# Kernel optimization log

Measured on AMD Instinct MI355X. Metric: run time of the kernel, lower is better.

## Reference

```python
import jax, jax.numpy as jnp
import numpy as np
import math

B, S, D = 8, 4096, 768
H = 12
DH = D // H  # attention_head_size = 64


def setup_inputs() -> dict:
    key = jax.random.key(0)
    ks = jax.random.split(key, 6)
    sc = 0.02
    return {
        "hidden_states": jax.random.normal(ks[0], (B, S, D), dtype=jnp.float32),
        "attention_mask": jnp.zeros((B, 1, S), dtype=jnp.float32),
        "Wq": jax.random.normal(ks[1], (D, D), dtype=jnp.float32) * sc,
        "bq": jnp.zeros((D,), dtype=jnp.float32),
        "Wqa": jax.random.normal(ks[2], (H, D), dtype=jnp.float32) * sc,
        "bqa": jnp.zeros((H,), dtype=jnp.float32),
        "Wk": jax.random.normal(ks[3], (D, D), dtype=jnp.float32) * sc,
        "bk": jnp.zeros((D,), dtype=jnp.float32),
        "Wt": jax.random.normal(ks[4], (D, D), dtype=jnp.float32) * sc,
        "bt": jnp.zeros((D,), dtype=jnp.float32),
    }


def reference(hidden_states, attention_mask, Wq, bq, Wqa, bqa, Wk, bk, Wt, bt):
    inv_sqrt_dh = 1.0 / math.sqrt(DH)
    # projections (torch nn.Linear: x @ W.T + b)
    q = hidden_states @ Wq.T + bq            # [B,S,D]
    k = hidden_states @ Wk.T + bk            # [B,S,D]
    # query attention logits -> [B,H,S]
    qfs = jnp.swapaxes(q @ Wqa.T + bqa, 1, 2) * inv_sqrt_dh + attention_mask
    qw = jax.nn.softmax(qfs, axis=-1)        # [B,H,S]
    ql = jnp.swapaxes(q.reshape(B, S, H, DH), 1, 2)  # [B,H,S,DH]
    kl = jnp.swapaxes(k.reshape(B, S, H, DH), 1, 2)  # [B,H,S,DH]
    # global pooled query per head
    pooled_q = jnp.einsum('bhs,bhsd->bhd', qw, ql)   # [B,H,DH]
    # key attention over pooled query
    qks = jnp.einsum('bhsd,bhd->bhs', kl, pooled_q) * inv_sqrt_dh + attention_mask
    qkw = jax.nn.softmax(qks, axis=-1)       # [B,H,S]
    pooled_k = jnp.einsum('bhs,bhsd->bhd', qkw, kl)  # [B,H,DH]
    # gate query with pooled key, merge heads
    wv = pooled_k[:, :, None, :] * ql        # [B,H,S,DH]
    wv = jnp.swapaxes(wv, 1, 2).reshape(B, S, D)
    return wv @ Wt.T + bt + q
```

## Files before the change

kernel.cpp:

```cpp
#include <hip/hip_runtime.h>
#include <cstdint>
#include <cstddef>

#define S_LEN 4096
#define NB 8
#define NH 12
#define DMODEL 768
#define DHEAD 64
#define M_TOT (NB * S_LEN)
#define INV_SQRT_DH 0.125f
#define WSZ (DMODEL * DMODEL)

typedef __attribute__((ext_vector_type(4))) float f32x4;
typedef __attribute__((ext_vector_type(8))) short bf16x8;

__device__ inline float bf2f(unsigned short h) {
    union { unsigned int u; float f; } v; v.u = ((unsigned int)h) << 16; return v.f;
}
__device__ inline unsigned short f2bf(float f) {
    union { float f; unsigned int u; } v; v.f = f;
    unsigned int r = v.u + 0x7FFFu + ((v.u >> 16) & 1u);
    return (unsigned short)(r >> 16);
}

__device__ inline void gload_lds16(const unsigned short* gp, void* lp) {
    __builtin_amdgcn_global_load_lds((const __attribute__((address_space(1))) void*)gp,
                                     (__attribute__((address_space(3))) void*)lp,
                                     16, 0, 0);
}

__global__ void prep_all(const float* __restrict__ hs,
                         const float* __restrict__ Wq, const float* __restrict__ Wk,
                         const float* __restrict__ Wt, const float* __restrict__ Wqa,
                         const float* __restrict__ bq, const float* __restrict__ bk,
                         unsigned short* __restrict__ hs_bf,
                         unsigned short* __restrict__ Wqk_bf, unsigned short* __restrict__ Wt_bf,
                         unsigned short* __restrict__ Wqa_bf, float* __restrict__ bqk) {
    int bid = blockIdx.x;
    int t = threadIdx.x;
    if (bid < 24576) {
        int off = bid * 1024 + t * 4;
        float4 v = *(const float4*)(hs + off);
        ushort4 o;
        o.x = f2bf(v.x); o.y = f2bf(v.y); o.z = f2bf(v.z); o.w = f2bf(v.w);
        *(ushort4*)(hs_bf + off) = o;
        return;
    }
    bid -= 24576;
    if (bid < 1728) {
        const float* src = (bid < 576) ? Wq : ((bid < 1152) ? Wk : Wt);
        unsigned short* dst = (bid < 576) ? Wqk_bf : ((bid < 1152) ? (Wqk_bf + WSZ) : Wt_bf);
        int off = (bid % 576) * 1024 + t * 4;
        float4 v = *(const float4*)(src + off);
        ushort4 o;
        o.x = f2bf(v.x); o.y = f2bf(v.y); o.z = f2bf(v.z); o.w = f2bf(v.w);
        *(ushort4*)(dst + off) = o;
    } else if (bid < 1740) {
        int off = (bid - 1728) * 1024 + t * 4;
        int h = off / DMODEL;
        ushort4 o = {0, 0, 0, 0};
        if (h < NH) {
            float4 v = *(const float4*)(Wqa + off);
            o.x = f2bf(v.x); o.y = f2bf(v.y); o.z = f2bf(v.z); o.w = f2bf(v.w);
        }
        *(ushort4*)(Wqa_bf + off) = o;
    } else {
        int off = (bid - 1740) * 1024 + t * 4;
        if (off < 2 * DMODEL) {
            const float* src = (off < DMODEL) ? (bq + off) : (bk + off - DMODEL);
            *(float4*)(bqk + off) = *(const float4*)src;
        }
    }
}

#define PH_MID() do { __builtin_amdgcn_s_barrier(); \
    asm volatile("s_waitcnt lgkmcnt(0)"); \
    __builtin_amdgcn_sched_barrier(0); \
    __builtin_amdgcn_s_setprio(1); } while (0)
#define PH_END() do { __builtin_amdgcn_s_setprio(0); \
    __builtin_amdgcn_s_barrier(); } while (0)

#define STG_A(q, kt, BO) gload_lds16(pA + (size_t)((q) * 64) * 768 + (kt) * 64, \
                                     lds + (BO) + (q) * 8192 + wOff)
#define STG_B(q, kt, BO) gload_lds16(pB + (size_t)((q) * 64) * 768 + (kt) * 64, \
                                     lds + (BO) + 32768 + (q) * 8192 + wOff)

#define LD_A(mh, BO) do { _Pragma("unroll") for (int mm = 0; mm < 4; ++mm) { \
    a[mm][0] = *(const bf16x8*)(lds + (BO) + aRd0 + ((mh) * 4 + mm) * 2048); \
    a[mm][1] = *(const bf16x8*)(lds + (BO) + aRd1 + ((mh) * 4 + mm) * 2048); } } while (0)
#define LD_B(nh, BO) do { _Pragma("unroll") for (int nn = 0; nn < 2; ++nn) { \
    b[(nh) * 2 + nn][0] = *(const bf16x8*)(lds + (BO) + bRd0 + ((nh) * 2 + nn) * 2048); \
    b[(nh) * 2 + nn][1] = *(const bf16x8*)(lds + (BO) + bRd1 + ((nh) * 2 + nn) * 2048); } } while (0)
#define MFMAQ(mh, nh) do { _Pragma("unroll") for (int mm = 0; mm < 4; ++mm) \
    _Pragma("unroll") for (int nn = 0; nn < 2; ++nn) { \
        acc[(mh) * 4 + mm][(nh) * 2 + nn] = __builtin_amdgcn_mfma_f32_16x16x32_bf16( \
            a[mm][0], b[(nh) * 2 + nn][0], acc[(mh) * 4 + mm][(nh) * 2 + nn], 0, 0, 0); \
        acc[(mh) * 4 + mm][(nh) * 2 + nn] = __builtin_amdgcn_mfma_f32_16x16x32_bf16( \
            a[mm][1], b[(nh) * 2 + nn][1], acc[(mh) * 4 + mm][(nh) * 2 + nn], 0, 0, 0); } } while (0)

__global__ __launch_bounds__(512, 2) void gemm8(
    const unsigned short* __restrict__ A,
    const unsigned short* __restrict__ Bw,
    const float* __restrict__ bias,
    unsigned short* __restrict__ outBf, int ldoBf,
    int ntn)
{
    __shared__ __align__(16) char lds[131072];

    int nwg = gridDim.x;
    int bid = blockIdx.x;
    int cpx = nwg >> 3;
    int swz = (bid & 7) * cpx + (bid >> 3);
    int bidn = swz % ntn, bidm = swz / ntn;
    int m0 = bidm * 256, n0 = bidn * 256;

    int t = threadIdx.x;
    int w = t >> 6, lane = t & 63;
    int lr = lane & 15, lk = lane >> 4;
    int wr = w >> 2, wc = w & 3;
    int wOff = w << 10;

    int srow = t >> 3;
    int sblk = (t & 7) ^ (srow & 7);
    const unsigned short* pA = A + (size_t)(m0 + srow) * 768 + sblk * 8;
    const unsigned short* pB = Bw + (size_t)(n0 + srow) * 768 + sblk * 8;

    int sx = lr & 7;
    int aRd0 = (wr * 128 + lr) * 128 + ((0 + lk) ^ sx) * 16;
    int aRd1 = (wr * 128 + lr) * 128 + ((4 + lk) ^ sx) * 16;
    int bRd0 = 32768 + (wc * 64 + lr) * 128 + ((0 + lk) ^ sx) * 16;
    int bRd1 = 32768 + (wc * 64 + lr) * 128 + ((4 + lk) ^ sx) * 16;

    f32x4 acc[8][4];
#pragma unroll
    for (int m = 0; m < 8; ++m)
#pragma unroll
        for (int n = 0; n < 4; ++n)
            acc[m][n] = (f32x4){0.f, 0.f, 0.f, 0.f};
    bf16x8 a[4][2], b[4][2];

    STG_A(0, 0, 0); STG_A(1, 0, 0); STG_A(2, 0, 0); STG_A(3, 0, 0);
    STG_B(0, 0, 0); STG_B(1, 0, 0); STG_B(2, 0, 0); STG_B(3, 0, 0);
    STG_A(0, 1, 65536); STG_A(2, 1, 65536);
    STG_B(0, 1, 65536); STG_B(1, 1, 65536); STG_B(2, 1, 65536); STG_B(3, 1, 65536);
    asm volatile("s_waitcnt vmcnt(6)");
    __builtin_amdgcn_s_barrier();

    for (int i = 0; i < 6; ++i) {
        int ktE = 2 * i, ktO = 2 * i + 1;
        int s2 = (i < 5);
        LD_A(0, 0); LD_B(0, 0);
        STG_A(1, ktO, 65536); STG_A(3, ktO, 65536);
        PH_MID(); MFMAQ(0, 0); PH_END();
        LD_B(1, 0);
        if (s2) { STG_A(0, ktE + 2, 0); STG_A(2, ktE + 2, 0); }
        PH_MID(); MFMAQ(0, 1); PH_END();
        LD_A(1, 0);
        if (s2) { STG_B(0, ktE + 2, 0); STG_B(1, ktE + 2, 0); }
        PH_MID(); MFMAQ(1, 1); PH_END();
        if (s2) { STG_B(2, ktE + 2, 0); STG_B(3, ktE + 2, 0); }
        PH_MID(); MFMAQ(1, 0);
        __builtin_amdgcn_s_setprio(0);
        if (s2) { asm volatile("s_waitcnt vmcnt(6)"); }
        else    { asm volatile("s_waitcnt vmcnt(0)"); }
        __builtin_amdgcn_s_barrier();
        LD_A(0, 65536); LD_B(0, 65536);
        if (s2) { STG_A(1, ktE + 2, 0); STG_A(3, ktE + 2, 0); }
        PH_MID(); MFMAQ(0, 0); PH_END();
        LD_B(1, 65536);
        if (s2) { STG_A(0, ktO + 2, 65536); STG_A(2, ktO + 2, 65536); }
        PH_MID(); MFMAQ(0, 1); PH_END();
        LD_A(1, 65536);
        if (s2) { STG_B(0, ktO + 2, 65536); STG_B(1, ktO + 2, 65536); }
        PH_MID(); MFMAQ(1, 1); PH_END();
        if (s2) { STG_B(2, ktO + 2, 65536); STG_B(3, ktO + 2, 65536); }
        PH_MID(); MFMAQ(1, 0);
        __builtin_amdgcn_s_setprio(0);
        if (s2) { asm volatile("s_waitcnt vmcnt(6)"); }
        __builtin_amdgcn_s_barrier();
    }

#pragma unroll
    for (int m = 0; m < 8; ++m) {
        int gr0 = m0 + wr * 128 + m * 16 + lk * 4;
#pragma unroll
        for (int n = 0; n < 4; ++n) {
            int gc = n0 + wc * 64 + n * 16 + lr;
            float bv = bias[gc];
#pragma unroll
            for (int r = 0; r < 4; ++r) {
                int gr = gr0 + r;
                outBf[(size_t)gr * ldoBf + gc] = f2bf(acc[m][n][r] + bv);
            }
        }
    }
}

#define STG3_A(q, kt, BO) gload_lds16(pA + (size_t)((q) * 64) * 1536 + (kt) * 64, \
                                      lds + (BO) + (q) * 8192 + wOff)
#define STG3_B(q, kt, BO) gload_lds16(pB + (size_t)((q) * 64) * 768 + (kt) * 64, \
                                      lds + (BO) + 32768 + (q) * 8192 + wOff)
#define LD3_A(mlo, BO) do { _Pragma("unroll") for (int mm = 0; mm < 4; ++mm) { \
    a[mm][0] = *(const bf16x8*)(lds + (BO) + aRd0 + ((mlo) + mm) * 2048); \
    a[mm][1] = *(const bf16x8*)(lds + (BO) + aRd1 + ((mlo) + mm) * 2048); } } while (0)
#define LD3_B(BO) do { _Pragma("unroll") for (int nn = 0; nn < 2; ++nn) { \
    b[nn][0] = *(const bf16x8*)(lds + (BO) + bRd0 + (nn) * 2048); \
    b[nn][1] = *(const bf16x8*)(lds + (BO) + bRd1 + (nn) * 2048); } } while (0)
#define MFMA3(mlo) do { _Pragma("unroll") for (int mm = 0; mm < 4; ++mm) \
    _Pragma("unroll") for (int nn = 0; nn < 2; ++nn) { \
        acc[(mlo) + mm][nn] = __builtin_amdgcn_mfma_f32_16x16x32_bf16( \
            a[mm][0], b[nn][0], acc[(mlo) + mm][nn], 0, 0, 0); \
        acc[(mlo) + mm][nn] = __builtin_amdgcn_mfma_f32_16x16x32_bf16( \
            a[mm][1], b[nn][1], acc[(mlo) + mm][nn], 0, 0, 0); } } while (0)

#define TILE3(t, BO, SO) do { \
    int t2 = (t) + 2; int s2 = (t2 < 12); \
    LD3_A(0, BO); LD3_B(BO); \
    if (s2) { STG3_A(0, t2, SO); STG3_A(1, t2, SO); STG3_A(2, t2, SO); } \
    PH_MID(); MFMA3(0); PH_END(); \
    LD3_A(4, BO); \
    if (s2) { STG3_A(3, t2, SO); STG3_B(0, t2, SO); STG3_B(1, t2, SO); } \
    PH_MID(); MFMA3(4); \
    __builtin_amdgcn_s_setprio(0); \
    if ((t) <= 9) { asm volatile("s_waitcnt vmcnt(6)"); } \
    else if ((t) == 10) { asm volatile("s_waitcnt vmcnt(0)"); } \
    __builtin_amdgcn_s_barrier(); \
} while (0)

__global__ __launch_bounds__(512, 2) void gemm8b(
    const unsigned short* __restrict__ A,
    const unsigned short* __restrict__ W8,
    const float* __restrict__ bias,
    float* __restrict__ outF,
    const unsigned short* __restrict__ resid)
{
    __shared__ __align__(16) char lds[147456];

    int nwg = gridDim.x;
    int bid = blockIdx.x;
    int cpx = nwg >> 3;
    int swz = (bid & 7) * cpx + (bid >> 3);
    int bidn = swz % 6, bidm = swz / 6;
    int m0 = bidm * 256, n0 = bidn * 128;

    const unsigned short* Bw = W8 + (size_t)(m0 >> 12) * WSZ;

    int t = threadIdx.x;
    int w = t >> 6, lane = t & 63;
    int lr = lane & 15, lk = lane >> 4;
    int wr = w >> 2, wc = w & 3;
    int wOff = w << 10;

    int srow = t >> 3;
    int sblk = (t & 7) ^ (srow & 7);
    const unsigned short* pA = A + (size_t)(m0 + srow) * 1536 + sblk * 8;
    const unsigned short* pB = Bw + (size_t)(n0 + srow) * 768 + sblk * 8;

    int sx = lr & 7;
    int aRd0 = (wr * 128 + lr) * 128 + ((0 + lk) ^ sx) * 16;
    int aRd1 = (wr * 128 + lr) * 128 + ((4 + lk) ^ sx) * 16;
    int bRd0 = 32768 + (wc * 32 + lr) * 128 + ((0 + lk) ^ sx) * 16;
    int bRd1 = 32768 + (wc * 32 + lr) * 128 + ((4 + lk) ^ sx) * 16;

    f32x4 acc[8][2];
#pragma unroll
    for (int m = 0; m < 8; ++m)
#pragma unroll
        for (int n = 0; n < 2; ++n)
            acc[m][n] = (f32x4){0.f, 0.f, 0.f, 0.f};
    bf16x8 a[4][2], b[2][2];

    STG3_A(0, 0, 0); STG3_A(1, 0, 0); STG3_A(2, 0, 0); STG3_A(3, 0, 0);
    STG3_B(0, 0, 0); STG3_B(1, 0, 0);
    STG3_A(0, 1, 49152); STG3_A(1, 1, 49152); STG3_A(2, 1, 49152); STG3_A(3, 1, 49152);
    STG3_B(0, 1, 49152); STG3_B(1, 1, 49152);
    asm volatile("s_waitcnt vmcnt(6)");
    __builtin_amdgcn_s_barrier();

    for (int ii = 0; ii < 4; ++ii) {
        int tb = ii * 3;
        TILE3(tb + 0, 0,     98304);
        TILE3(tb + 1, 49152, 0);
        TILE3(tb + 2, 98304, 49152);
    }

#pragma unroll
    for (int m = 0; m < 8; ++m) {
        int gr0 = m0 + wr * 128 + m * 16 + lk * 4;
#pragma unroll
        for (int n = 0; n < 2; ++n) {
            int gc = n0 + wc * 32 + n * 16 + lr;
            float bv = bias[gc];
#pragma unroll
            for (int r = 0; r < 4; ++r) {
                int gr = gr0 + r;
                float v = acc[m][n][r] + bv + bf2f(resid[(size_t)gr * 1536 + gc]);
                outF[(size_t)gr * DMODEL + gc] = v;
            }
        }
    }
}

__global__ __launch_bounds__(256) void qfs_kernel(
    const unsigned short* __restrict__ q, int ldq,
    const unsigned short* __restrict__ wqa,
    const float* __restrict__ bqa,
    const float* __restrict__ mask,
    float* __restrict__ qfs)
{
    int t = threadIdx.x;
    int w = t >> 6, lane = t & 63;
    int lr = lane & 15, lk = lane >> 4;
    int m0 = blockIdx.x * 64 + w * 16;

    f32x4 acc = (f32x4){0.f, 0.f, 0.f, 0.f};
    for (int k0 = 0; k0 < DMODEL; k0 += 32) {
        bf16x8 av = *(const bf16x8*)&q[(size_t)(m0 + lr) * ldq + k0 + lk * 8];
        bf16x8 bv = *(const bf16x8*)&wqa[lr * DMODEL + k0 + lk * 8];
        acc = __builtin_amdgcn_mfma_f32_16x16x32_bf16(av, bv, acc, 0, 0, 0);
    }
    if (lr < NH) {
        float bv = bqa[lr];
#pragma unroll
        for (int r = 0; r < 4; ++r) {
            int m = m0 + lk * 4 + r;
            int b_ = m >> 12;
            int s = m & (S_LEN - 1);
            qfs[((size_t)b_ * NH + lr) * S_LEN + s] = acc[r] * INV_SQRT_DH + bv + mask[b_ * S_LEN + s];
        }
    }
}

__global__ __launch_bounds__(256) void pool1_kernel(
    const float* __restrict__ logits,
    const unsigned short* __restrict__ qk,
    float* __restrict__ parts)
{
    int bid = blockIdx.x;
    int bh = bid >> 3, c = bid & 7;
    int b = bh / NH, h = bh % NH;
    int s0 = c * 512;
    int t = threadIdx.x;

    __shared__ float w[512];
    __shared__ float red[8];
    __shared__ float part[4][64];

    const float* lg = logits + (size_t)bh * S_LEN + s0;
    float l0 = lg[t], l1 = lg[t + 256];
    float m = fmaxf(l0, l1);
#pragma unroll
    for (int off = 32; off; off >>= 1) m = fmaxf(m, __shfl_xor(m, off));
    if ((t & 63) == 0) red[t >> 6] = m;
    __syncthreads();
    float M = fmaxf(fmaxf(red[0], red[1]), fmaxf(red[2], red[3]));
    float w0 = __expf(l0 - M), w1 = __expf(l1 - M);
    w[t] = w0; w[t + 256] = w1;
    float z = w0 + w1;
#pragma unroll
    for (int off = 32; off; off >>= 1) z += __shfl_xor(z, off);
    if ((t & 63) == 0) red[4 + (t >> 6)] = z;
    __syncthreads();
    float Z = red[4] + red[5] + red[6] + red[7];

    int dblk = t & 7, rgrp = t >> 3;
    const unsigned short* xp = qk + ((size_t)(b * S_LEN + s0)) * 1536 + h * DHEAD + dblk * 8;
    float acc[8];
#pragma unroll
    for (int e = 0; e < 8; ++e) acc[e] = 0.f;
    for (int j = 0; j < 16; ++j) {
        int r = j * 32 + rgrp;
        bf16x8 v = *(const bf16x8*)(xp + (size_t)r * 1536);
        float wr = w[r];
#pragma unroll
        for (int e = 0; e < 8; ++e) acc[e] += wr * bf2f((unsigned short)v[e]);
    }
#pragma unroll
    for (int off = 8; off <= 32; off <<= 1)
#pragma unroll
        for (int e = 0; e < 8; ++e) acc[e] += __shfl_xor(acc[e], off);
    if ((t & 63) < 8) {
#pragma unroll
        for (int e = 0; e < 8; ++e) part[t >> 6][(t & 7) * 8 + e] = acc[e];
    }
    __syncthreads();
    float* dst = parts + ((size_t)bh * 8 + c) * 72;
    if (t < 64) dst[t] = part[0][t] + part[1][t] + part[2][t] + part[3][t];
    else if (t == 64) dst[64] = M;
    else if (t == 65) dst[65] = Z;
}

__global__ __launch_bounds__(256) void pool2_kernel(
    const float* __restrict__ parts1,
    const unsigned short* __restrict__ qk,
    const float* __restrict__ mask,
    float* __restrict__ parts2)
{
    int bid = blockIdx.x;
    int bh = bid >> 3, c = bid & 7;
    int b = bh / NH, h = bh % NH;
    int s0 = c * 512;
    int t = threadIdx.x;

    __shared__ float pq[64];
    __shared__ float w[512];
    __shared__ float red[8];
    __shared__ float part[4][64];

    if (t < 64) {
        const float* p1 = parts1 + (size_t)bh * 8 * 72;
        float M1 = -1e30f;
#pragma unroll
        for (int cc = 0; cc < 8; ++cc) M1 = fmaxf(M1, p1[cc * 72 + 64]);
        float Z1 = 0.f, a1 = 0.f;
#pragma unroll
        for (int cc = 0; cc < 8; ++cc) {
            float f = __expf(p1[cc * 72 + 64] - M1);
            Z1 += f * p1[cc * 72 + 65];
            a1 += f * p1[cc * 72 + t];
        }
        pq[t] = a1 / Z1;
    }
    __syncthreads();

    int dblk = t & 7, rgrp = t >> 3;
    float pq8[8];
#pragma unroll
    for (int e = 0; e < 8; ++e) pq8[e] = pq[dblk * 8 + e];

    const unsigned short* kp = qk + ((size_t)(b * S_LEN + s0)) * 1536 + DMODEL + h * DHEAD + dblk * 8;

    for (int j = 0; j < 16; ++j) {
        int r = j * 32 + rgrp;
        bf16x8 v = *(const bf16x8*)(kp + (size_t)r * 1536);
        float d = 0.f;
#pragma unroll
        for (int e = 0; e < 8; ++e) d += bf2f((unsigned short)v[e]) * pq8[e];
        d += __shfl_xor(d, 1); d += __shfl_xor(d, 2); d += __shfl_xor(d, 4);
        if (dblk == 0) w[r] = d * INV_SQRT_DH + mask[b * S_LEN + s0 + r];
    }
    __syncthreads();

    float l0 = w[t], l1 = w[t + 256];
    float m = fmaxf(l0, l1);
#pragma unroll
    for (int off = 32; off; off >>= 1) m = fmaxf(m, __shfl_xor(m, off));
    if ((t & 63) == 0) red[t >> 6] = m;
    __syncthreads();
    float M = fmaxf(fmaxf(red[0], red[1]), fmaxf(red[2], red[3]));
    float w0 = __expf(l0 - M), w1 = __expf(l1 - M);
    float z = w0 + w1;
#pragma unroll
    for (int off = 32; off; off >>= 1) z += __shfl_xor(z, off);
    if ((t & 63) == 0) red[4 + (t >> 6)] = z;
    __syncthreads();
    w[t] = w0; w[t + 256] = w1;
    __syncthreads();
    float Z = red[4] + red[5] + red[6] + red[7];

    float acc[8];
#pragma unroll
    for (int e = 0; e < 8; ++e) acc[e] = 0.f;
    for (int j = 0; j < 16; ++j) {
        int r = j * 32 + rgrp;
        bf16x8 v = *(const bf16x8*)(kp + (size_t)r * 1536);
        float wr = w[r];
#pragma unroll
        for (int e = 0; e < 8; ++e) acc[e] += wr * bf2f((unsigned short)v[e]);
    }
#pragma unroll
    for (int off = 8; off <= 32; off <<= 1)
#pragma unroll
        for (int e = 0; e < 8; ++e) acc[e] += __shfl_xor(acc[e], off);
    if ((t & 63) < 8) {
#pragma unroll
        for (int e = 0; e < 8; ++e) part[t >> 6][(t & 7) * 8 + e] = acc[e];
    }
    __syncthreads();
    float* dst = parts2 + ((size_t)bh * 8 + c) * 72;
    if (t < 64) dst[t] = part[0][t] + part[1][t] + part[2][t] + part[3][t];
    else if (t == 64) dst[64] = M;
    else if (t == 65) dst[65] = Z;
}

__global__ __launch_bounds__(256) void gatedw_kernel(
    const float* __restrict__ parts2,
    const unsigned short* __restrict__ Wt_bf,
    unsigned short* __restrict__ W8)
{
    int bid = blockIdx.x;
    int b = bid / 96, rg = bid % 96;
    int t = threadIdx.x;

    __shared__ float mhc[96], Mh[12], fac[96], zh[12], pk[768];

    if (t < 96) mhc[t] = parts2[((size_t)(b * NH + t / 8) * 8 + (t & 7)) * 72 + 64];
    __syncthreads();
    if (t < 12) {
        float M = -1e30f;
#pragma unroll
        for (int cc = 0; cc < 8; ++cc) M = fmaxf(M, mhc[t * 8 + cc]);
        Mh[t] = M;
    }
    __syncthreads();
    if (t < 96) fac[t] = __expf(mhc[t] - Mh[t / 8]);
    __syncthreads();
    if (t < 12) {
        float Zm = 0.f;
#pragma unroll
        for (int cc = 0; cc < 8; ++cc)
            Zm += fac[t * 8 + cc] * parts2[((size_t)(b * NH + t) * 8 + cc) * 72 + 65];
        zh[t] = Zm;
    }
    __syncthreads();
#pragma unroll
    for (int j = 0; j < 3; ++j) {
        int col = t + 256 * j;
        int h = col >> 6, d = col & 63;
        const float* p2 = parts2 + (size_t)(b * NH + h) * 8 * 72;
        float v = 0.f;
#pragma unroll
        for (int cc = 0; cc < 8; ++cc) v += fac[h * 8 + cc] * p2[cc * 72 + d];
        pk[col] = v / zh[h];
    }
    __syncthreads();
#pragma unroll
    for (int j = 0; j < 3; ++j) {
        int idx = j * 2048 + t * 8;
        int r = rg * 8 + idx / DMODEL, k = idx % DMODEL;
        bf16x8 wv = *(const bf16x8*)(Wt_bf + (size_t)r * DMODEL + k);
        bf16x8 o;
#pragma unroll
        for (int e = 0; e < 8; ++e)
            o[e] = (short)f2bf(bf2f((unsigned short)wv[e]) * pk[k + e]);
        *(bf16x8*)(W8 + (size_t)b * WSZ + (size_t)r * DMODEL + k) = o;
    }
}

extern "C" void kernel_launch(void* const* d_in, const int* in_sizes, int n_in,
                              void* d_out, int out_size, void* d_ws, size_t ws_size,
                              hipStream_t stream) {
    const float* hs   = (const float*)d_in[0];
    const float* mask = (const float*)d_in[1];
    const float* Wq   = (const float*)d_in[2];
    const float* bq   = (const float*)d_in[3];
    const float* Wqa  = (const float*)d_in[4];
    const float* bqa  = (const float*)d_in[5];
    const float* Wk   = (const float*)d_in[6];
    const float* bk   = (const float*)d_in[7];
    const float* Wt   = (const float*)d_in[8];
    const float* bt   = (const float*)d_in[9];
    float* out = (float*)d_out;

    char* ws = (char*)d_ws;
    unsigned short* qk_bf  = (unsigned short*)(ws);
    unsigned short* hs_bf  = (unsigned short*)(ws + 100663296);
    unsigned short* W8     = hs_bf;
    unsigned short* Wqk_bf = (unsigned short*)(ws + 150994944);
    unsigned short* Wt_bf  = (unsigned short*)(ws + 153354240);
    unsigned short* Wqa_bf = (unsigned short*)(ws + 154533888);
    float* bqk    = (float*)(ws + 154558464);
    float* qfs    = (float*)(ws + 154564608);
    float* parts1 = (float*)(ws + 156137472);
    float* parts2 = (float*)(ws + 156358656);

    prep_all<<<26318, 256, 0, stream>>>(hs, Wq, Wk, Wt, Wqa, bq, bk,
                                        hs_bf, Wqk_bf, Wt_bf, Wqa_bf, bqk);

    gemm8<<<(M_TOT / 256) * 6, 512, 0, stream>>>(
        hs_bf, Wqk_bf, bqk, qk_bf, 2 * DMODEL, 6);

    qfs_kernel<<<M_TOT / 64, 256, 0, stream>>>(qk_bf, 2 * DMODEL, Wqa_bf, bqa, mask, qfs);
    pool1_kernel<<<NB * NH * 8, 256, 0, stream>>>(qfs, qk_bf, parts1);
    pool2_kernel<<<NB * NH * 8, 256, 0, stream>>>(parts1, qk_bf, mask, parts2);
    gatedw_kernel<<<NB * 96, 256, 0, stream>>>(parts2, Wt_bf, W8);

    gemm8b<<<(M_TOT / 256) * 6, 512, 0, stream>>>(
        qk_bf, W8, bt, out, qk_bf);
}
```

Before: 215.6 us.

## Shrink final output GEMM tile to 128x64 with 256-thread blocks

The final Wt GEMM (with bias and residual add) moves from 256x128 tiles on 512-thread blocks to 128x64 tiles on 256-thread blocks. Grid size grows fourfold, LDS per block halves to 72KB, and the staging and MFMA macros are rewritten for the smaller per-wave footprint. The aim is more blocks and better occupancy and load balance across CUs. The cost is lower data reuse per tile, so more global and L2 traffic for A and W.

```diff
diff --git a/kernel.cpp b/kernel.cpp
--- a/kernel.cpp
+++ b/kernel.cpp
@@ -196,60 +196,58 @@
     }
 }
 
-#define STG3_A(q, kt, BO) gload_lds16(pA + (size_t)((q) * 64) * 1536 + (kt) * 64, \
-                                      lds + (BO) + (q) * 8192 + wOff)
-#define STG3_B(q, kt, BO) gload_lds16(pB + (size_t)((q) * 64) * 768 + (kt) * 64, \
-                                      lds + (BO) + 32768 + (q) * 8192 + wOff)
-#define LD3_A(mlo, BO) do { _Pragma("unroll") for (int mm = 0; mm < 4; ++mm) { \
-    a[mm][0] = *(const bf16x8*)(lds + (BO) + aRd0 + ((mlo) + mm) * 2048); \
-    a[mm][1] = *(const bf16x8*)(lds + (BO) + aRd1 + ((mlo) + mm) * 2048); } } while (0)
-#define LD3_B(BO) do { _Pragma("unroll") for (int nn = 0; nn < 2; ++nn) { \
-    b[nn][0] = *(const bf16x8*)(lds + (BO) + bRd0 + (nn) * 2048); \
-    b[nn][1] = *(const bf16x8*)(lds + (BO) + bRd1 + (nn) * 2048); } } while (0)
-#define MFMA3(mlo) do { _Pragma("unroll") for (int mm = 0; mm < 4; ++mm) \
-    _Pragma("unroll") for (int nn = 0; nn < 2; ++nn) { \
-        acc[(mlo) + mm][nn] = __builtin_amdgcn_mfma_f32_16x16x32_bf16( \
-            a[mm][0], b[nn][0], acc[(mlo) + mm][nn], 0, 0, 0); \
-        acc[(mlo) + mm][nn] = __builtin_amdgcn_mfma_f32_16x16x32_bf16( \
-            a[mm][1], b[nn][1], acc[(mlo) + mm][nn], 0, 0, 0); } } while (0)
-
-#define TILE3(t, BO, SO) do { \
-    int t2 = (t) + 2; int s2 = (t2 < 12); \
-    LD3_A(0, BO); LD3_B(BO); \
-    if (s2) { STG3_A(0, t2, SO); STG3_A(1, t2, SO); STG3_A(2, t2, SO); } \
-    PH_MID(); MFMA3(0); PH_END(); \
-    LD3_A(4, BO); \
-    if (s2) { STG3_A(3, t2, SO); STG3_B(0, t2, SO); STG3_B(1, t2, SO); } \
-    PH_MID(); MFMA3(4); \
+#define STG5_A(q, kt, SB) gload_lds16(pA + (size_t)((q) * 32) * 1536 + (kt) * 64, \
+                                      lds + (SB) + (q) * 4096 + tOff)
+#define STG5_B(q, kt, SB) gload_lds16(pB + (size_t)((q) * 32) * 768 + (kt) * 64, \
+                                      lds + (SB) + 16384 + (q) * 4096 + tOff)
+#define LD5(ARD, BRD, BUF) do { _Pragma("unroll") for (int mm = 0; mm < 4; ++mm) \
+        a[mm] = *(const bf16x8*)(lds + (BUF) + (ARD) + mm * 2048); \
+    _Pragma("unroll") for (int nn = 0; nn < 2; ++nn) \
+        b[nn] = *(const bf16x8*)(lds + (BUF) + (BRD) + nn * 2048); } while (0)
+#define MFMA5() do { _Pragma("unroll") for (int mm = 0; mm < 4; ++mm) \
+    _Pragma("unroll") for (int nn = 0; nn < 2; ++nn) \
+        acc[mm][nn] = __builtin_amdgcn_mfma_f32_16x16x32_bf16( \
+            a[mm], b[nn], acc[mm][nn], 0, 0, 0); } while (0)
+
+#define TILE5(t, BUF, SB) do { \
+     \
+    LD5(aRd0, bRd0, BUF); \
+    if ((t) <= 9) { STG5_A(0, (t) + 2, SB); STG5_A(1, (t) + 2, SB); \
+                    STG5_A(2, (t) + 2, SB); STG5_A(3, (t) + 2, SB); } \
+    PH_MID(); MFMA5(); PH_END(); \
+     \
+    LD5(aRd1, bRd1, BUF); \
+    if ((t) <= 9) { STG5_B(0, (t) + 2, SB); STG5_B(1, (t) + 2, SB); } \
+    PH_MID(); MFMA5(); \
     __builtin_amdgcn_s_setprio(0); \
-    if ((t) <= 9) { asm volatile("s_waitcnt vmcnt(6)"); } \
+    if ((t) <= 9)       { asm volatile("s_waitcnt vmcnt(6)"); } \
     else if ((t) == 10) { asm volatile("s_waitcnt vmcnt(0)"); } \
     __builtin_amdgcn_s_barrier(); \
 } while (0)
 
-__global__ __launch_bounds__(512, 2) void gemm8b(
+__global__ __launch_bounds__(256, 2) void gemm2k(
     const unsigned short* __restrict__ A,
     const unsigned short* __restrict__ W8,
     const float* __restrict__ bias,
     float* __restrict__ outF,
     const unsigned short* __restrict__ resid)
 {
-    __shared__ __align__(16) char lds[147456];
+    __shared__ __align__(16) char lds[73728];
 
     int nwg = gridDim.x;
     int bid = blockIdx.x;
     int cpx = nwg >> 3;
     int swz = (bid & 7) * cpx + (bid >> 3);
-    int bidn = swz % 6, bidm = swz / 6;
-    int m0 = bidm * 256, n0 = bidn * 128;
+    int bidn = swz % 12, bidm = swz / 12;
+    int m0 = bidm * 128, n0 = bidn * 64;
 
     const unsigned short* Bw = W8 + (size_t)(m0 >> 12) * WSZ;
 
     int t = threadIdx.x;
     int w = t >> 6, lane = t & 63;
     int lr = lane & 15, lk = lane >> 4;
-    int wr = w >> 2, wc = w & 3;
-    int wOff = w << 10;
+    int wr = w >> 1, wc = w & 1;
+    int tOff = w << 10;
 
     int srow = t >> 3;
     int sblk = (t & 7) ^ (srow & 7);
@@ -257,36 +255,36 @@
     const unsigned short* pB = Bw + (size_t)(n0 + srow) * 768 + sblk * 8;
 
     int sx = lr & 7;
-    int aRd0 = (wr * 128 + lr) * 128 + ((0 + lk) ^ sx) * 16;
-    int aRd1 = (wr * 128 + lr) * 128 + ((4 + lk) ^ sx) * 16;
-    int bRd0 = 32768 + (wc * 32 + lr) * 128 + ((0 + lk) ^ sx) * 16;
-    int bRd1 = 32768 + (wc * 32 + lr) * 128 + ((4 + lk) ^ sx) * 16;
-
-    f32x4 acc[8][2];
-#pragma unroll
-    for (int m = 0; m < 8; ++m)
+    int aRd0 = (wr * 64 + lr) * 128 + ((0 + lk) ^ sx) * 16;
+    int aRd1 = (wr * 64 + lr) * 128 + ((4 + lk) ^ sx) * 16;
+    int bRd0 = 16384 + (wc * 32 + lr) * 128 + ((0 + lk) ^ sx) * 16;
+    int bRd1 = 16384 + (wc * 32 + lr) * 128 + ((4 + lk) ^ sx) * 16;
+
+    f32x4 acc[4][2];
+#pragma unroll
+    for (int m = 0; m < 4; ++m)
 #pragma unroll
         for (int n = 0; n < 2; ++n)
             acc[m][n] = (f32x4){0.f, 0.f, 0.f, 0.f};
-    bf16x8 a[4][2], b[2][2];
-
-    STG3_A(0, 0, 0); STG3_A(1, 0, 0); STG3_A(2, 0, 0); STG3_A(3, 0, 0);
-    STG3_B(0, 0, 0); STG3_B(1, 0, 0);
-    STG3_A(0, 1, 49152); STG3_A(1, 1, 49152); STG3_A(2, 1, 49152); STG3_A(3, 1, 49152);
-    STG3_B(0, 1, 49152); STG3_B(1, 1, 49152);
+    bf16x8 a[4], b[2];
+
+    STG5_A(0, 0, 0); STG5_A(1, 0, 0); STG5_A(2, 0, 0); STG5_A(3, 0, 0);
+    STG5_B(0, 0, 0); STG5_B(1, 0, 0);
+    STG5_A(0, 1, 24576); STG5_A(1, 1, 24576); STG5_A(2, 1, 24576); STG5_A(3, 1, 24576);
+    STG5_B(0, 1, 24576); STG5_B(1, 1, 24576);
     asm volatile("s_waitcnt vmcnt(6)");
     __builtin_amdgcn_s_barrier();
 
     for (int ii = 0; ii < 4; ++ii) {
         int tb = ii * 3;
-        TILE3(tb + 0, 0,     98304);
-        TILE3(tb + 1, 49152, 0);
-        TILE3(tb + 2, 98304, 49152);
-    }
-
-#pragma unroll
-    for (int m = 0; m < 8; ++m) {
-        int gr0 = m0 + wr * 128 + m * 16 + lk * 4;
+        TILE5(tb + 0, 0,     49152);
+        TILE5(tb + 1, 24576, 0);
+        TILE5(tb + 2, 49152, 24576);
+    }
+
+#pragma unroll
+    for (int m = 0; m < 4; ++m) {
+        int gr0 = m0 + wr * 64 + m * 16 + lk * 4;
 #pragma unroll
         for (int n = 0; n < 2; ++n) {
             int gc = n0 + wc * 32 + n * 16 + lr;
@@ -575,6 +573,6 @@
     pool2_kernel<<<NB * NH * 8, 256, 0, stream>>>(parts1, qk_bf, mask, parts2);
     gatedw_kernel<<<NB * 96, 256, 0, stream>>>(parts2, Wt_bf, W8);
 
-    gemm8b<<<(M_TOT / 256) * 6, 512, 0, stream>>>(
+    gemm2k<<<(M_TOT / 128) * 12, 256, 0, stream>>>(
         qk_bf, W8, bt, out, qk_bf);
 }
```

Measured after the change: 213.4 us. Within noise of the previous version (-1.0%).
